# Performance work log

Measured on AMD Instinct MI355X. Metric: run time of the kernel, lower is better.

The kernel has to match this reference:

```python
import jax, jax.numpy as jnp
import numpy as np
import math

D_MODEL = 2048
N_HEADS = 16
HEAD_DIM = D_MODEL // N_HEADS  # 128
SEQ_LEN = 4096
BATCH = 4


def rotate_half(x):
    x1, x2 = x[..., : x.shape[-1] // 2], x[..., x.shape[-1] // 2 :]
    return jnp.concatenate((-x2, x1), axis=-1)


def rope_cos_sin(seq_len, head_dim, dtype=jnp.float32):
    inv_freq = 1.0 / (10000.0 ** (jnp.arange(0, head_dim, 2, dtype=jnp.float32) / head_dim))
    freqs = jnp.arange(seq_len, dtype=jnp.float32)[:, None] * inv_freq[None, :]  # [S, D/2]
    emb = jnp.concatenate((freqs, freqs), axis=-1)  # [S, D]
    return jnp.cos(emb).astype(dtype), jnp.sin(emb).astype(dtype)


def setup_inputs() -> dict:
    key = jax.random.key(0)
    kx, kq, kk, kv = jax.random.split(key, 4)
    x = jax.random.normal(kx, (BATCH, SEQ_LEN, D_MODEL), dtype=jnp.float32)
    s = 1.0 / math.sqrt(D_MODEL)
    # torch Linear weight: [out_features, in_features]
    w_q = jax.random.uniform(kq, (HEAD_DIM, D_MODEL), minval=-s, maxval=s, dtype=jnp.float32)
    w_k = jax.random.uniform(kk, (HEAD_DIM, D_MODEL), minval=-s, maxval=s, dtype=jnp.float32)
    w_v = jax.random.uniform(kv, (HEAD_DIM, D_MODEL), minval=-s, maxval=s, dtype=jnp.float32)
    return {"x": x, "w_q": w_q, "w_k": w_k, "w_v": w_v}


def reference(x, w_q, w_k, w_v):
    B, S, _ = x.shape
    scale = 1.0 / math.sqrt(HEAD_DIM)
    # projections: x @ W^T  -> [B, S, head_dim]
    q = jnp.einsum('bsd,hd->bsh', x, w_q)
    k = jnp.einsum('bsd,hd->bsh', x, w_k)
    v = jnp.einsum('bsd,hd->bsh', x, w_v)
    cos, sin = rope_cos_sin(S, HEAD_DIM, x.dtype)  # [S, head_dim]
    q = q * cos + rotate_half(q) * sin
    k = k * cos + rotate_half(k) * sin
    scores = jnp.einsum('bqh,bkh->bqk', q, k) * scale  # [B, S, S]
    causal = jnp.tril(jnp.ones((S, S), dtype=bool))
    scores = jnp.where(causal[None, :, :], scores, -jnp.inf)
    attn = jax.nn.softmax(scores, axis=-1)
    out = jnp.einsum('bqk,bkh->bqh', attn, v)  # [B, S, head_dim]
    return out
```

## Files before the change

### kernel.cpp

```cpp
#include <hip/hip_runtime.h>
#include <hip/hip_bf16.h>

#define BATCH 4
#define SEQ 4096
#define DMODEL 2048
#define HD 128
#define BS (BATCH*SEQ)

typedef __attribute__((ext_vector_type(8))) short short8;
typedef __attribute__((ext_vector_type(4))) float f32x4;
typedef __attribute__((ext_vector_type(4))) float float4v;
typedef unsigned short u16;
typedef unsigned int u32;

#define LOG2E 1.4426950408889634f
#define SCALE 0.08838834764831845f

__device__ __forceinline__ u16 f2bf(float f){
  u32 u = __builtin_bit_cast(u32, f);
  u32 r = (u + 0x7FFFu + ((u >> 16) & 1u)) >> 16;
  return (u16)r;
}

__device__ __forceinline__ void gload16(const void* gptr, void* lptr){
  __builtin_amdgcn_global_load_lds((const __attribute__((address_space(1))) void*)gptr,
                                   (__attribute__((address_space(3))) void*)lptr, 16, 0, 0);
}

__global__ __launch_bounds__(256) void k_tab(float2* __restrict__ tab){
  int i = blockIdx.x*256 + threadIdx.x;
  int s = i >> 6, j = i & 63;
  float invf = (float)pow(10000.0, -(double)j/64.0);
  float ang  = (float)s * invf;
  double a = (double)ang;
  tab[i] = make_float2((float)cos(a), (float)sin(a));
}

__global__ __launch_bounds__(256) void k_cvtw(const float* __restrict__ wq, const float* __restrict__ wk,
                                              const float* __restrict__ wv, u16* __restrict__ wb){
  int i = blockIdx.x*256 + threadIdx.x;
  int m = i >> 18; int r = i & 262143;
  const float* s = (m==0) ? wq : ((m==1) ? wk : wv);
  wb[i] = f2bf(s[r]);
}

__global__ __launch_bounds__(256) void k_gemm(
    const float* __restrict__ x, const u16* __restrict__ wb, const float2* __restrict__ tab,
    u16* __restrict__ qb, u16* __restrict__ kb, u16* __restrict__ vt)
{
  __shared__ char lds[2][65536];
  const int tid = threadIdx.x;
  const size_t M0 = (size_t)blockIdx.x * 64;
  const int w = tid >> 6, lane = tid & 63, lr = lane & 15, lg = lane >> 4;
  const int h = w & 1, g = w >> 1;

  int nfs[6];
  nfs[0] = g*8 + 2*h;     nfs[1] = nfs[0] + 4;
  nfs[2] = g*8 + 2*h + 1; nfs[3] = nfs[2] + 4;
  nfs[4] = 16 + 2*w;      nfs[5] = nfs[4] + 1;

  int aoff[4], adst[4], woff[12], wdst[12];
  #pragma unroll
  for (int i=0;i<4;i++){
    int L = i*4096 + tid*16;
    int row = L >> 8, cb = L & 255;
    int scb = cb ^ ((row & 7) << 5);
    aoff[i] = (int)((M0 + row)*DMODEL) + (scb >> 2);
    adst[i] = L;
  }
  #pragma unroll
  for (int i=0;i<12;i++){
    int L = i*4096 + tid*16;
    int row = L >> 7, cb = L & 127;
    int scb = cb ^ ((row & 7) << 4);
    woff[i] = row*DMODEL + (scb >> 1);
    wdst[i] = 16384 + L;
  }

  f32x4 acc[4][6];
  #pragma unroll
  for (int i=0;i<4;i++)
    #pragma unroll
    for (int j=0;j<6;j++) acc[i][j] = f32x4{0.f,0.f,0.f,0.f};

  {
    char* base = lds[0];
    #pragma unroll
    for (int i=0;i<4;i++)  gload16(x + aoff[i], base + adst[i]);
    #pragma unroll
    for (int i=0;i<12;i++) gload16(wb + woff[i], base + wdst[i]);
  }
  __syncthreads();

  int cur = 0;
  for (int t=0; t<32; t++){
    if (t < 31){
      char* base = lds[cur^1];
      const int k0 = (t+1)*64;
      #pragma unroll
      for (int i=0;i<4;i++)  gload16(x + aoff[i] + k0, base + adst[i]);
      #pragma unroll
      for (int i=0;i<12;i++) gload16(wb + woff[i] + k0, base + wdst[i]);
    }
    const char* lA = lds[cur];
    const char* lW = lds[cur] + 16384;

    short8 af[2][4];
    #pragma unroll
    for (int ks=0;ks<2;ks++)
      #pragma unroll
      for (int rf=0;rf<4;rf++){
        int r = rf*16 + lr;
        int byte = r*256 + ((ks*128 + lg*32) ^ ((r&7)<<5));
        f32x4 va = *(const f32x4*)(lA + byte);
        f32x4 vb = *(const f32x4*)(lA + byte + 16);
        short8 tt;
        tt[0]=(short)f2bf(va[0]); tt[1]=(short)f2bf(va[1]); tt[2]=(short)f2bf(va[2]); tt[3]=(short)f2bf(va[3]);
        tt[4]=(short)f2bf(vb[0]); tt[5]=(short)f2bf(vb[1]); tt[6]=(short)f2bf(vb[2]); tt[7]=(short)f2bf(vb[3]);
        af[ks][rf] = tt;
      }
    #pragma unroll
    for (int j=0;j<6;j++){
      int rw = nfs[j]*16 + lr;
      #pragma unroll
      for (int ks=0;ks<2;ks++){
        int byte = rw*128 + ((ks*64 + lg*16) ^ ((lr&7)<<4));
        short8 bf = *(const short8*)(lW + byte);
        #pragma unroll
        for (int rf=0;rf<4;rf++)
          acc[rf][j] = __builtin_amdgcn_mfma_f32_16x16x32_bf16(af[ks][rf], bf, acc[rf][j], 0,0,0);
      }
    }
    __syncthreads();
    cur ^= 1;
  }

  u16* dst = (g == 0) ? qb : kb;
  #pragma unroll
  for (int rf=0; rf<4; rf++)
    #pragma unroll
    for (int reg=0; reg<4; reg++){
      size_t grow = M0 + rf*16 + lg*4 + reg;
      int spos = (int)(grow & (SEQ-1));
      size_t b = grow >> 12;
      #pragma unroll
      for (int p=0; p<2; p++){
        int j = (2*h + p)*16 + lr;
        float2 cs = tab[spos*64 + j];
        float lo = acc[rf][2*p][reg];
        float hi = acc[rf][2*p+1][reg];
        dst[grow*HD + j]      = f2bf(lo*cs.x - hi*cs.y);
        dst[grow*HD + j + 64] = f2bf(hi*cs.x + lo*cs.y);
      }
      #pragma unroll
      for (int jj=0; jj<2; jj++){
        int col = (2*w + jj)*16 + lr;
        vt[(b*HD + col)*SEQ + spos] = f2bf(acc[rf][4+jj][reg]);
      }
    }
}

__global__ __launch_bounds__(256) void k_attn(
    const u16* __restrict__ qbuf, const u16* __restrict__ kb, const u16* __restrict__ vt,
    float* __restrict__ Opart, float2* __restrict__ ml)
{
  __shared__ u16 lK[64*128];
  __shared__ u16 lV[128*64];
  __shared__ u16 lP[4][16*64];
  const int tid = threadIdx.x;
  const int bid = blockIdx.x;
  const int x = bid & 7, idx = bid >> 3;
  const int b = x >> 1, half = x & 1;
  const int qt = 63 - (idx >> 1);
  const int sp = (idx & 1) + 2*half;
  const int qbn = b*64 + qt;
  const int w = tid >> 6, lane = tid & 63, lr = lane & 15, lg = lane >> 4;

  const int n = qt + 1, cbase = n >> 2, crem = n & 3;
  const int cnt = cbase + (sp < crem ? 1 : 0);
  const int klo = sp*cbase + (sp < crem ? sp : crem);
  const int khi = klo + cnt;
  const size_t prow0 = ((size_t)qbn*4 + sp)*64;

  if (cnt == 0){
    if (lr == 0){
      #pragma unroll
      for (int reg=0; reg<4; reg++)
        ml[prow0 + w*16 + lg*4 + reg] = make_float2(-1e30f, 0.f);
    }
    return;
  }

  const size_t qrow = (size_t)b*SEQ + qt*64 + w*16 + lr;
  short8 aq[4];
  #pragma unroll
  for (int ks=0; ks<4; ks++)
    aq[ks] = *(const short8*)(qbuf + qrow*HD + ks*32 + lg*8);

  f32x4 accO[8];
  #pragma unroll
  for (int i=0;i<8;i++) accO[i] = f32x4{0.f,0.f,0.f,0.f};
  float m2[4]   = {-1e30f,-1e30f,-1e30f,-1e30f};
  float lsum[4] = {0.f,0.f,0.f,0.f};

  const int Lb = tid*16;
  const float cfac = SCALE * LOG2E;

  for (int kt = klo; kt < khi; kt++){
    #pragma unroll
    for (int i=0;i<4;i++){
      int L = i*4096 + Lb;
      { int row = L >> 8, cb = L & 255;
        int scb = cb ^ ((row & 7) << 4);
        gload16(kb + ((size_t)b*SEQ + kt*64 + row)*HD + (scb>>1), ((char*)lK) + L); }
      { int row = L >> 7, cb = L & 127;
        int scb = cb ^ ((row & 7) << 4);
        gload16(vt + ((size_t)b*HD + row)*SEQ + kt*64 + (scb>>1), ((char*)lV) + L); }
    }
    __syncthreads();

    f32x4 sc[4];
    #pragma unroll
    for (int nf=0; nf<4; nf++){
      sc[nf] = f32x4{0.f,0.f,0.f,0.f};
      #pragma unroll
      for (int ks=0; ks<4; ks++){
        int r = nf*16 + lr;
        int byte = r*256 + ((ks*64 + lg*16) ^ ((r&7)<<4));
        short8 bk = *(const short8*)((const char*)lK + byte);
        sc[nf] = __builtin_amdgcn_mfma_f32_16x16x32_bf16(aq[ks], bk, sc[nf], 0,0,0);
      }
      sc[nf] *= cfac;
    }
    if (kt == qt){
      #pragma unroll
      for (int nf=0; nf<4; nf++)
        #pragma unroll
        for (int reg=0; reg<4; reg++){
          int col = nf*16 + lr;
          int row = w*16 + lg*4 + reg;
          if (col > row) sc[nf][reg] = -1e30f;
        }
    }
    float al[4];
    #pragma unroll
    for (int reg=0; reg<4; reg++){
      float v = fmaxf(fmaxf(sc[0][reg], sc[1][reg]), fmaxf(sc[2][reg], sc[3][reg]));
      v = fmaxf(v, __shfl_xor(v, 1));
      v = fmaxf(v, __shfl_xor(v, 2));
      v = fmaxf(v, __shfl_xor(v, 4));
      v = fmaxf(v, __shfl_xor(v, 8));
      float mnew = fmaxf(m2[reg], v);
      al[reg] = exp2f(m2[reg] - mnew);
      m2[reg] = mnew;
    }
    float prs[4] = {0.f,0.f,0.f,0.f};
    #pragma unroll
    for (int nf=0; nf<4; nf++)
      #pragma unroll
      for (int reg=0; reg<4; reg++){
        float p = exp2f(sc[nf][reg] - m2[reg]);
        prs[reg] += p;
        int r = lg*4 + reg;
        int byte = r*128 + ((nf*32 + lr*2) ^ ((r&7)<<4));
        *(u16*)(((char*)lP[w]) + byte) = f2bf(p);
      }
    f32x4 alv = f32x4{al[0], al[1], al[2], al[3]};
    #pragma unroll
    for (int reg=0; reg<4; reg++){
      float v = prs[reg];
      v += __shfl_xor(v, 1);
      v += __shfl_xor(v, 2);
      v += __shfl_xor(v, 4);
      v += __shfl_xor(v, 8);
      lsum[reg] = lsum[reg]*al[reg] + v;
    }
    #pragma unroll
    for (int cf=0; cf<8; cf++) accO[cf] *= alv;

    short8 pa[2];
    #pragma unroll
    for (int ks=0; ks<2; ks++){
      int byte = lr*128 + ((ks*64 + lg*16) ^ ((lr&7)<<4));
      pa[ks] = *(const short8*)(((const char*)lP[w]) + byte);
    }
    #pragma unroll
    for (int cf=0; cf<8; cf++){
      #pragma unroll
      for (int ks=0; ks<2; ks++){
        int d = cf*16 + lr;
        int byte = d*128 + ((ks*64 + lg*16) ^ ((d&7)<<4));
        short8 bv = *(const short8*)(((const char*)lV) + byte);
        accO[cf] = __builtin_amdgcn_mfma_f32_16x16x32_bf16(pa[ks], bv, accO[cf], 0,0,0);
      }
    }
    __syncthreads();
  }

  #pragma unroll
  for (int reg=0; reg<4; reg++){
    size_t pr = prow0 + w*16 + lg*4 + reg;
    #pragma unroll
    for (int cf=0; cf<8; cf++)
      Opart[pr*HD + cf*16 + lr] = accO[cf][reg];
  }
  if (lr == 0){
    #pragma unroll
    for (int reg=0; reg<4; reg++)
      ml[prow0 + w*16 + lg*4 + reg] = make_float2(m2[reg], lsum[reg]);
  }
}

__global__ __launch_bounds__(256) void k_comb(
    const float* __restrict__ Opart, const float2* __restrict__ ml, float* __restrict__ out)
{
  const int t = threadIdx.x;
  const int r = blockIdx.x*8 + (t >> 5);
  const int c = (t & 31)*4;
  const int qbn = r >> 6, rr = r & 63;
  float m[4], l[4], M = -1e30f;
  #pragma unroll
  for (int s=0; s<4; s++){
    float2 v = ml[((size_t)qbn*4 + s)*64 + rr];
    m[s] = v.x; l[s] = v.y;
    M = fmaxf(M, m[s]);
  }
  float L = 0.f;
  #pragma unroll
  for (int s=0; s<4; s++){ m[s] = exp2f(m[s] - M); L += l[s]*m[s]; }
  const float inv = 1.0f / L;
  f32x4 acc = f32x4{0.f,0.f,0.f,0.f};
  #pragma unroll
  for (int s=0; s<4; s++){
    f32x4 o = *(const f32x4*)(Opart + (((size_t)qbn*4 + s)*64 + rr)*(size_t)HD + c);
    float sc = m[s]*inv;
    acc += o * sc;
  }
  *(f32x4*)(out + (size_t)r*HD + c) = acc;
}

extern "C" void kernel_launch(void* const* d_in, const int* in_sizes, int n_in,
                              void* d_out, int out_size, void* d_ws, size_t ws_size,
                              hipStream_t stream){
  const float* x  = (const float*)d_in[0];
  const float* wq = (const float*)d_in[1];
  const float* wk = (const float*)d_in[2];
  const float* wv = (const float*)d_in[3];
  float* out = (float*)d_out;
  char* ws = (char*)d_ws;

  size_t off = 0;
  u16* wb = (u16*)(ws + off); off += (size_t)3*HD*DMODEL*2;
  float2* tab = (float2*)(ws + off); off += (size_t)SEQ*64*8;
  u16* qb = (u16*)(ws + off); off += (size_t)BS*HD*2;
  u16* kb = (u16*)(ws + off); off += (size_t)BS*HD*2;
  u16* vt = (u16*)(ws + off); off += (size_t)BS*HD*2;
  float* Opart = (float*)(ws + off); off += (size_t)1024*64*HD*4;
  float2* ml   = (float2*)(ws + off); off += (size_t)1024*64*8;
  if (ws_size < off) return;

  hipLaunchKernelGGL(k_tab,  dim3(1024),  dim3(256), 0, stream, tab);
  hipLaunchKernelGGL(k_cvtw, dim3(3072),  dim3(256), 0, stream, wq, wk, wv, wb);
  hipLaunchKernelGGL(k_gemm, dim3(256),   dim3(256), 0, stream, x, wb, tab, qb, kb, vt);
  hipLaunchKernelGGL(k_attn, dim3(1024),  dim3(256), 0, stream, qb, kb, vt, Opart, ml);
  hipLaunchKernelGGL(k_comb, dim3(2048),  dim3(256), 0, stream, Opart, ml, out);
}
```

Baseline: 130.1 us.

## Halve GEMM row tile, convert x to bf16 in registers, prefetch through registers

```diff
diff --git a/kernel.cpp b/kernel.cpp
--- a/kernel.cpp
+++ b/kernel.cpp
@@ -48,9 +48,9 @@
     const float* __restrict__ x, const u16* __restrict__ wb, const float2* __restrict__ tab,
     u16* __restrict__ qb, u16* __restrict__ kb, u16* __restrict__ vt)
 {
-  __shared__ char lds[2][65536];
+  __shared__ char lds[8192 + 49152];
   const int tid = threadIdx.x;
-  const size_t M0 = (size_t)blockIdx.x * 64;
+  const size_t M0 = (size_t)blockIdx.x * 32;
   const int w = tid >> 6, lane = tid & 63, lr = lane & 15, lg = lane >> 4;
   const int h = w & 1, g = w >> 1;
 
@@ -59,85 +59,126 @@
   nfs[2] = g*8 + 2*h + 1; nfs[3] = nfs[2] + 4;
   nfs[4] = 16 + 2*w;      nfs[5] = nfs[4] + 1;
 
-  int aoff[4], adst[4], woff[12], wdst[12];
-  #pragma unroll
-  for (int i=0;i<4;i++){
-    int L = i*4096 + tid*16;
-    int row = L >> 8, cb = L & 255;
-    int scb = cb ^ ((row & 7) << 5);
-    aoff[i] = (int)((M0 + row)*DMODEL) + (scb >> 2);
-    adst[i] = L;
-  }
+  const int arow = tid >> 3, acol = (tid & 7)*8;
+  const float* axp = x + (M0 + arow)*DMODEL + acol;
+  const int awbyte = arow*128 + ((acol*2) ^ ((arow & 7) << 4));
+
+  int woff[12], wdst[12];
   #pragma unroll
   for (int i=0;i<12;i++){
     int L = i*4096 + tid*16;
     int row = L >> 7, cb = L & 127;
     int scb = cb ^ ((row & 7) << 4);
     woff[i] = row*DMODEL + (scb >> 1);
-    wdst[i] = 16384 + L;
-  }
-
-  f32x4 acc[4][6];
-  #pragma unroll
-  for (int i=0;i<4;i++)
+    wdst[i] = 8192 + L;
+  }
+
+  f32x4 acc[2][6];
+  #pragma unroll
+  for (int i=0;i<2;i++)
     #pragma unroll
     for (int j=0;j<6;j++) acc[i][j] = f32x4{0.f,0.f,0.f,0.f};
 
+  float4v s0a, s0b, s1a, s1b;
+
+  s0a = *(const float4v*)(axp);      s0b = *(const float4v*)(axp + 4);
+  __builtin_amdgcn_sched_barrier(0);
+  #pragma unroll
+  for (int i=0;i<12;i++) gload16(wb + woff[i], lds + wdst[i]);
+  __builtin_amdgcn_sched_barrier(0);
+  s1a = *(const float4v*)(axp + 64); s1b = *(const float4v*)(axp + 68);
+  __builtin_amdgcn_sched_barrier(0);
   {
-    char* base = lds[0];
-    #pragma unroll
-    for (int i=0;i<4;i++)  gload16(x + aoff[i], base + adst[i]);
-    #pragma unroll
-    for (int i=0;i<12;i++) gload16(wb + woff[i], base + wdst[i]);
-  }
-  __syncthreads();
-
-  int cur = 0;
-  for (int t=0; t<32; t++){
-    if (t < 31){
-      char* base = lds[cur^1];
-      const int k0 = (t+1)*64;
-      #pragma unroll
-      for (int i=0;i<4;i++)  gload16(x + aoff[i] + k0, base + adst[i]);
-      #pragma unroll
-      for (int i=0;i<12;i++) gload16(wb + woff[i] + k0, base + wdst[i]);
-    }
-    const char* lA = lds[cur];
-    const char* lW = lds[cur] + 16384;
-
-    short8 af[2][4];
+    short8 o;
+    o[0]=(short)f2bf(s0a[0]); o[1]=(short)f2bf(s0a[1]); o[2]=(short)f2bf(s0a[2]); o[3]=(short)f2bf(s0a[3]);
+    o[4]=(short)f2bf(s0b[0]); o[5]=(short)f2bf(s0b[1]); o[6]=(short)f2bf(s0b[2]); o[7]=(short)f2bf(s0b[3]);
+    *(short8*)(lds + awbyte) = o;
+  }
+  __builtin_amdgcn_sched_barrier(0);
+  asm volatile("s_waitcnt vmcnt(2) lgkmcnt(0)" ::: "memory");
+  __builtin_amdgcn_sched_barrier(0);
+  __builtin_amdgcn_s_barrier();
+  __builtin_amdgcn_sched_barrier(0);
+
+  for (int t=0; t<31; t++){
+    const int p = t & 1;
+    {
+      const char* lA = lds + p*4096;
+      const char* lW = lds + 8192;
+      short8 af[2][2];
+      #pragma unroll
+      for (int ks=0;ks<2;ks++)
+        #pragma unroll
+        for (int rf=0;rf<2;rf++){
+          int r = rf*16 + lr;
+          af[ks][rf] = *(const short8*)(lA + r*128 + ((ks*64 + lg*16) ^ ((r&7)<<4)));
+        }
+      #pragma unroll
+      for (int j=0;j<6;j++){
+        int rw = nfs[j]*16 + lr;
+        #pragma unroll
+        for (int ks=0;ks<2;ks++){
+          short8 bf = *(const short8*)(lW + rw*128 + ((ks*64 + lg*16) ^ ((lr&7)<<4)));
+          #pragma unroll
+          for (int rf=0;rf<2;rf++)
+            acc[rf][j] = __builtin_amdgcn_mfma_f32_16x16x32_bf16(af[ks][rf], bf, acc[rf][j], 0,0,0);
+        }
+      }
+    }
+    __builtin_amdgcn_sched_barrier(0);
+    __builtin_amdgcn_s_barrier();
+    __builtin_amdgcn_sched_barrier(0);
+    const int k0 = (t+1)*64;
+    #pragma unroll
+    for (int i=0;i<12;i++) gload16(wb + woff[i] + k0, lds + wdst[i]);
+    __builtin_amdgcn_sched_barrier(0);
+    {
+      const float* ap = axp + (t+2 <= 31 ? (t+2)*64 : 31*64);
+      float4v na = *(const float4v*)(ap), nb = *(const float4v*)(ap + 4);
+      if (p == 0){ s0a = na; s0b = nb; } else { s1a = na; s1b = nb; }
+    }
+    __builtin_amdgcn_sched_barrier(0);
+    {
+      float4v ca, cb2;
+      if (p == 0){ ca = s1a; cb2 = s1b; } else { ca = s0a; cb2 = s0b; }
+      short8 o;
+      o[0]=(short)f2bf(ca[0]);  o[1]=(short)f2bf(ca[1]);  o[2]=(short)f2bf(ca[2]);  o[3]=(short)f2bf(ca[3]);
+      o[4]=(short)f2bf(cb2[0]); o[5]=(short)f2bf(cb2[1]); o[6]=(short)f2bf(cb2[2]); o[7]=(short)f2bf(cb2[3]);
+      *(short8*)(lds + (p^1)*4096 + awbyte) = o;
+    }
+    __builtin_amdgcn_sched_barrier(0);
+    asm volatile("s_waitcnt vmcnt(2) lgkmcnt(0)" ::: "memory");
+    __builtin_amdgcn_sched_barrier(0);
+    __builtin_amdgcn_s_barrier();
+    __builtin_amdgcn_sched_barrier(0);
+  }
+  {
+    const char* lA = lds + (31 & 1)*4096;
+    const char* lW = lds + 8192;
+    short8 af[2][2];
     #pragma unroll
     for (int ks=0;ks<2;ks++)
       #pragma unroll
-      for (int rf=0;rf<4;rf++){
+      for (int rf=0;rf<2;rf++){
         int r = rf*16 + lr;
-        int byte = r*256 + ((ks*128 + lg*32) ^ ((r&7)<<5));
-        f32x4 va = *(const f32x4*)(lA + byte);
-        f32x4 vb = *(const f32x4*)(lA + byte + 16);
-        short8 tt;
-        tt[0]=(short)f2bf(va[0]); tt[1]=(short)f2bf(va[1]); tt[2]=(short)f2bf(va[2]); tt[3]=(short)f2bf(va[3]);
-        tt[4]=(short)f2bf(vb[0]); tt[5]=(short)f2bf(vb[1]); tt[6]=(short)f2bf(vb[2]); tt[7]=(short)f2bf(vb[3]);
-        af[ks][rf] = tt;
+        af[ks][rf] = *(const short8*)(lA + r*128 + ((ks*64 + lg*16) ^ ((r&7)<<4)));
       }
     #pragma unroll
     for (int j=0;j<6;j++){
       int rw = nfs[j]*16 + lr;
       #pragma unroll
       for (int ks=0;ks<2;ks++){
-        int byte = rw*128 + ((ks*64 + lg*16) ^ ((lr&7)<<4));
-        short8 bf = *(const short8*)(lW + byte);
+        short8 bf = *(const short8*)(lW + rw*128 + ((ks*64 + lg*16) ^ ((lr&7)<<4)));
         #pragma unroll
-        for (int rf=0;rf<4;rf++)
+        for (int rf=0;rf<2;rf++)
           acc[rf][j] = __builtin_amdgcn_mfma_f32_16x16x32_bf16(af[ks][rf], bf, acc[rf][j], 0,0,0);
       }
     }
-    __syncthreads();
-    cur ^= 1;
   }
 
   u16* dst = (g == 0) ? qb : kb;
   #pragma unroll
-  for (int rf=0; rf<4; rf++)
+  for (int rf=0; rf<2; rf++)
     #pragma unroll
     for (int reg=0; reg<4; reg++){
       size_t grow = M0 + rf*16 + lg*4 + reg;
@@ -361,7 +402,7 @@
 
   hipLaunchKernelGGL(k_tab,  dim3(1024),  dim3(256), 0, stream, tab);
   hipLaunchKernelGGL(k_cvtw, dim3(3072),  dim3(256), 0, stream, wq, wk, wv, wb);
-  hipLaunchKernelGGL(k_gemm, dim3(256),   dim3(256), 0, stream, x, wb, tab, qb, kb, vt);
+  hipLaunchKernelGGL(k_gemm, dim3(512),   dim3(256), 0, stream, x, wb, tab, qb, kb, vt);
   hipLaunchKernelGGL(k_attn, dim3(1024),  dim3(256), 0, stream, qb, kb, vt, Opart, ml);
   hipLaunchKernelGGL(k_comb, dim3(2048),  dim3(256), 0, stream, Opart, ml, out);
 }
```

Result: no change. 127.7 us (-1.9%).

## Restructure projection GEMM: 128-row tiles, split N across blocks, convert x to bf16 once

Applied to the files above, without the earlier changes.

```diff
diff --git a/kernel.cpp b/kernel.cpp
--- a/kernel.cpp
+++ b/kernel.cpp
@@ -39,124 +39,140 @@
 __global__ __launch_bounds__(256) void k_cvtw(const float* __restrict__ wq, const float* __restrict__ wk,
                                               const float* __restrict__ wv, u16* __restrict__ wb){
   int i = blockIdx.x*256 + threadIdx.x;
-  int m = i >> 18; int r = i & 262143;
-  const float* s = (m==0) ? wq : ((m==1) ? wk : wv);
-  wb[i] = f2bf(s[r]);
-}
-
-__global__ __launch_bounds__(256) void k_gemm(
+  int r = i >> 11, k = i & 2047;
+  const float* s; int sr;
+  if (r < 128)      { s = wq; sr = r; }
+  else if (r < 192) { s = wv; sr = r - 128; }
+  else if (r < 320) { s = wk; sr = r - 192; }
+  else              { s = wv; sr = r - 256; }
+  wb[i] = f2bf(s[sr*2048 + k]);
+}
+
+__global__ __launch_bounds__(512,2) void k_gemm(
     const float* __restrict__ x, const u16* __restrict__ wb, const float2* __restrict__ tab,
     u16* __restrict__ qb, u16* __restrict__ kb, u16* __restrict__ vt)
 {
-  __shared__ char lds[2][65536];
+  __shared__ char lds[81920];
   const int tid = threadIdx.x;
-  const size_t M0 = (size_t)blockIdx.x * 64;
+  const int bid = blockIdx.x;
+  const int xcd = bid & 7, li = bid >> 3;
+  const int mg = (li >> 1)*8 + xcd;
+  const int ng = li & 1;
+  const size_t M0 = (size_t)mg * 128;
   const int w = tid >> 6, lane = tid & 63, lr = lane & 15, lg = lane >> 4;
-  const int h = w & 1, g = w >> 1;
-
-  int nfs[6];
-  nfs[0] = g*8 + 2*h;     nfs[1] = nfs[0] + 4;
-  nfs[2] = g*8 + 2*h + 1; nfs[3] = nfs[2] + 4;
-  nfs[4] = 16 + 2*w;      nfs[5] = nfs[4] + 1;
-
-  int aoff[4], adst[4], woff[12], wdst[12];
-  #pragma unroll
-  for (int i=0;i<4;i++){
-    int L = i*4096 + tid*16;
-    int row = L >> 8, cb = L & 255;
-    int scb = cb ^ ((row & 7) << 5);
-    aoff[i] = (int)((M0 + row)*DMODEL) + (scb >> 2);
-    adst[i] = L;
-  }
-  #pragma unroll
-  for (int i=0;i<12;i++){
-    int L = i*4096 + tid*16;
+  const int wm = w >> 2, wn = w & 3;
+
+  const int arow = tid >> 2, akq = (tid & 3)*16;
+  const float* axp = x + (M0 + arow)*DMODEL + akq;
+  const int asw  = (arow & 7) << 4;
+  const int awb0 = arow*128 + ((2*akq) ^ asw);
+  const int awb1 = arow*128 + ((2*akq + 16) ^ asw);
+
+  int woff[3], wdst[3];
+  #pragma unroll
+  for (int i=0;i<3;i++){
+    int L = i*8192 + tid*16;
     int row = L >> 7, cb = L & 127;
     int scb = cb ^ ((row & 7) << 4);
-    woff[i] = row*DMODEL + (scb >> 1);
-    wdst[i] = 16384 + L;
-  }
-
-  f32x4 acc[4][6];
+    woff[i] = (ng*192 + row)*DMODEL + (scb >> 1);
+    wdst[i] = 32768 + L;
+  }
+  const int slots[3] = {wn, wn+4, 8+wn};
+
+  f32x4 acc[4][3];
   #pragma unroll
   for (int i=0;i<4;i++)
     #pragma unroll
-    for (int j=0;j<6;j++) acc[i][j] = f32x4{0.f,0.f,0.f,0.f};
-
+    for (int j=0;j<3;j++) acc[i][j] = f32x4{0.f,0.f,0.f,0.f};
+
+  float4v a0, a1, a2, a3;
+
+  a0 = *(const float4v*)(axp);     a1 = *(const float4v*)(axp + 4);
+  a2 = *(const float4v*)(axp + 8); a3 = *(const float4v*)(axp + 12);
+  #pragma unroll
+  for (int i=0;i<3;i++) gload16(wb + woff[i], lds + wdst[i]);
   {
-    char* base = lds[0];
-    #pragma unroll
-    for (int i=0;i<4;i++)  gload16(x + aoff[i], base + adst[i]);
-    #pragma unroll
-    for (int i=0;i<12;i++) gload16(wb + woff[i], base + wdst[i]);
-  }
-  __syncthreads();
-
-  int cur = 0;
+    short8 o;
+    o[0]=(short)f2bf(a0[0]); o[1]=(short)f2bf(a0[1]); o[2]=(short)f2bf(a0[2]); o[3]=(short)f2bf(a0[3]);
+    o[4]=(short)f2bf(a1[0]); o[5]=(short)f2bf(a1[1]); o[6]=(short)f2bf(a1[2]); o[7]=(short)f2bf(a1[3]);
+    *(short8*)(lds + awb0) = o;
+    o[0]=(short)f2bf(a2[0]); o[1]=(short)f2bf(a2[1]); o[2]=(short)f2bf(a2[2]); o[3]=(short)f2bf(a2[3]);
+    o[4]=(short)f2bf(a3[0]); o[5]=(short)f2bf(a3[1]); o[6]=(short)f2bf(a3[2]); o[7]=(short)f2bf(a3[3]);
+    *(short8*)(lds + awb1) = o;
+  }
+  __builtin_amdgcn_sched_barrier(0);
+  asm volatile("s_waitcnt vmcnt(0) lgkmcnt(0)" ::: "memory");
+  __builtin_amdgcn_sched_barrier(0);
+  __builtin_amdgcn_s_barrier();
+  __builtin_amdgcn_sched_barrier(0);
+
   for (int t=0; t<32; t++){
+    const int p = t & 1;
     if (t < 31){
-      char* base = lds[cur^1];
+      const float* ap = axp + (t+1)*64;
+      a0 = *(const float4v*)(ap);     a1 = *(const float4v*)(ap + 4);
+      a2 = *(const float4v*)(ap + 8); a3 = *(const float4v*)(ap + 12);
       const int k0 = (t+1)*64;
       #pragma unroll
-      for (int i=0;i<4;i++)  gload16(x + aoff[i] + k0, base + adst[i]);
-      #pragma unroll
-      for (int i=0;i<12;i++) gload16(wb + woff[i] + k0, base + wdst[i]);
-    }
-    const char* lA = lds[cur];
-    const char* lW = lds[cur] + 16384;
-
-    short8 af[2][4];
-    #pragma unroll
-    for (int ks=0;ks<2;ks++)
-      #pragma unroll
-      for (int rf=0;rf<4;rf++){
-        int r = rf*16 + lr;
-        int byte = r*256 + ((ks*128 + lg*32) ^ ((r&7)<<5));
-        f32x4 va = *(const f32x4*)(lA + byte);
-        f32x4 vb = *(const f32x4*)(lA + byte + 16);
-        short8 tt;
-        tt[0]=(short)f2bf(va[0]); tt[1]=(short)f2bf(va[1]); tt[2]=(short)f2bf(va[2]); tt[3]=(short)f2bf(va[3]);
-        tt[4]=(short)f2bf(vb[0]); tt[5]=(short)f2bf(vb[1]); tt[6]=(short)f2bf(vb[2]); tt[7]=(short)f2bf(vb[3]);
-        af[ks][rf] = tt;
+      for (int i=0;i<3;i++) gload16(wb + woff[i] + k0, lds + wdst[i] + (p^1)*24576);
+    }
+    __builtin_amdgcn_sched_barrier(0);
+    {
+      const char* lA = lds + p*16384;
+      const char* lW = lds + p*24576;
+      short8 af[2][4];
+      #pragma unroll
+      for (int ks=0;ks<2;ks++)
+        #pragma unroll
+        for (int rf=0;rf<4;rf++){
+          int r = wm*64 + rf*16 + lr;
+          af[ks][rf] = *(const short8*)(lA + r*128 + ((ks*64 + lg*16) ^ ((r&7)<<4)));
+        }
+      #pragma unroll
+      for (int s=0;s<3;s++){
+        int lrow = slots[s]*16 + lr;
+        #pragma unroll
+        for (int ks=0;ks<2;ks++){
+          short8 wf = *(const short8*)(lW + 32768 + lrow*128 + ((ks*64 + lg*16) ^ ((lrow&7)<<4)));
+          #pragma unroll
+          for (int rf=0;rf<4;rf++)
+            acc[rf][s] = __builtin_amdgcn_mfma_f32_16x16x32_bf16(af[ks][rf], wf, acc[rf][s], 0,0,0);
+        }
       }
-    #pragma unroll
-    for (int j=0;j<6;j++){
-      int rw = nfs[j]*16 + lr;
-      #pragma unroll
-      for (int ks=0;ks<2;ks++){
-        int byte = rw*128 + ((ks*64 + lg*16) ^ ((lr&7)<<4));
-        short8 bf = *(const short8*)(lW + byte);
-        #pragma unroll
-        for (int rf=0;rf<4;rf++)
-          acc[rf][j] = __builtin_amdgcn_mfma_f32_16x16x32_bf16(af[ks][rf], bf, acc[rf][j], 0,0,0);
-      }
-    }
-    __syncthreads();
-    cur ^= 1;
-  }
-
-  u16* dst = (g == 0) ? qb : kb;
+    }
+    __builtin_amdgcn_sched_barrier(0);
+    if (t < 31){
+      short8 o;
+      o[0]=(short)f2bf(a0[0]); o[1]=(short)f2bf(a0[1]); o[2]=(short)f2bf(a0[2]); o[3]=(short)f2bf(a0[3]);
+      o[4]=(short)f2bf(a1[0]); o[5]=(short)f2bf(a1[1]); o[6]=(short)f2bf(a1[2]); o[7]=(short)f2bf(a1[3]);
+      *(short8*)(lds + (p^1)*16384 + awb0) = o;
+      o[0]=(short)f2bf(a2[0]); o[1]=(short)f2bf(a2[1]); o[2]=(short)f2bf(a2[2]); o[3]=(short)f2bf(a2[3]);
+      o[4]=(short)f2bf(a3[0]); o[5]=(short)f2bf(a3[1]); o[6]=(short)f2bf(a3[2]); o[7]=(short)f2bf(a3[3]);
+      *(short8*)(lds + (p^1)*16384 + awb1) = o;
+    }
+    __builtin_amdgcn_sched_barrier(0);
+    asm volatile("s_waitcnt vmcnt(0) lgkmcnt(0)" ::: "memory");
+    __builtin_amdgcn_sched_barrier(0);
+    __builtin_amdgcn_s_barrier();
+    __builtin_amdgcn_sched_barrier(0);
+  }
+
+  u16* dst = ng ? kb : qb;
   #pragma unroll
   for (int rf=0; rf<4; rf++)
     #pragma unroll
     for (int reg=0; reg<4; reg++){
-      size_t grow = M0 + rf*16 + lg*4 + reg;
+      size_t grow = M0 + wm*64 + rf*16 + lg*4 + reg;
       int spos = (int)(grow & (SEQ-1));
       size_t b = grow >> 12;
-      #pragma unroll
-      for (int p=0; p<2; p++){
-        int j = (2*h + p)*16 + lr;
-        float2 cs = tab[spos*64 + j];
-        float lo = acc[rf][2*p][reg];
-        float hi = acc[rf][2*p+1][reg];
-        dst[grow*HD + j]      = f2bf(lo*cs.x - hi*cs.y);
-        dst[grow*HD + j + 64] = f2bf(hi*cs.x + lo*cs.y);
-      }
-      #pragma unroll
-      for (int jj=0; jj<2; jj++){
-        int col = (2*w + jj)*16 + lr;
-        vt[(b*HD + col)*SEQ + spos] = f2bf(acc[rf][4+jj][reg]);
-      }
+      int j = wn*16 + lr;
+      float2 cs = tab[spos*64 + j];
+      float lo = acc[rf][0][reg];
+      float hi = acc[rf][1][reg];
+      dst[grow*HD + j]      = f2bf(lo*cs.x - hi*cs.y);
+      dst[grow*HD + j + 64] = f2bf(hi*cs.x + lo*cs.y);
+      int vcol = wn*16 + lr + ng*64;
+      vt[(b*HD + vcol)*SEQ + spos] = f2bf(acc[rf][2][reg]);
     }
 }
 
@@ -361,7 +377,7 @@
 
   hipLaunchKernelGGL(k_tab,  dim3(1024),  dim3(256), 0, stream, tab);
   hipLaunchKernelGGL(k_cvtw, dim3(3072),  dim3(256), 0, stream, wq, wk, wv, wb);
-  hipLaunchKernelGGL(k_gemm, dim3(256),   dim3(256), 0, stream, x, wb, tab, qb, kb, vt);
+  hipLaunchKernelGGL(k_gemm, dim3(256),   dim3(512), 0, stream, x, wb, tab, qb, kb, vt);
   hipLaunchKernelGGL(k_attn, dim3(1024),  dim3(256), 0, stream, qb, kb, vt, Opart, ml);
   hipLaunchKernelGGL(k_comb, dim3(2048),  dim3(256), 0, stream, Opart, ml, out);
 }
```

After: 116.4 us. 10.5% less time.
